# Kernel tuning notes

Measured on AMD Instinct MI355X. Metric: run time of the kernel, lower is better.

## Reference

```python
import jax, jax.numpy as jnp
import numpy as np


def setup_inputs() -> dict:
    key = jax.random.key(0)
    ks = jax.random.split(key, 6)
    D, k, r = 4096, 16, 32  # embed_dim, low_rank_dimension, 2*low_rank_dimension
    B, S = 4, 4096
    return {
        "base": jax.random.normal(ks[0], (B, S, D), dtype=jnp.float32),
        "lora_A": jax.random.normal(ks[1], (k, D), dtype=jnp.float32),
        "lora_E": jax.random.normal(ks[2], (r, 1), dtype=jnp.float32),
        "lora_B": jax.random.normal(ks[3], (r, k), dtype=jnp.float32),
        "lora_aa": jax.random.normal(ks[4], (k, r), dtype=jnp.float32),
        "lora_bb": jax.random.normal(ks[5], (D, k), dtype=jnp.float32),
    }


def reference(base, lora_A, lora_E, lora_B, lora_aa, lora_bb):
    # Original math: base + base @ (A.T @ B.T @ diag(E) @ aa.T @ bb.T)
    #   result1 = A.T @ B.T  -> [D, r]
    #   result2 = aa.T @ bb.T -> [r, D]
    # Efficient equivalent: keep it low-rank; never build the [D, D] matrix
    # or the explicit diag. diag(E) @ result2 == E * result2 (row scaling).
    e = lora_E.reshape(-1)                              # [r]
    t = jnp.einsum('bsd,kd->bsk', base, lora_A)         # [B,S,k]  (base @ A.T)
    t = jnp.einsum('bsk,rk->bsr', t, lora_B)            # [B,S,r]  (.. @ B.T)
    t = t * e                                           # diag(E) scaling
    t = jnp.einsum('bsr,kr->bsk', t, lora_aa)           # [B,S,k]  (.. @ aa.T)
    delta = jnp.einsum('bsk,dk->bsd', t, lora_bb)       # [B,S,D]  (.. @ bb.T)
    return (base + delta).astype(base.dtype)
```

## Files before the change

### kernel.cpp

```cpp
#include <hip/hip_runtime.h>
#include <hip/hip_bf16.h>


#define D_DIM 4096
#define K_LR 16
#define R_LR 32
#define ROWS 64
#define NW 16
#define WWIN 256
#define DC 32
#define NCH (WWIN / DC)

typedef float f32x4 __attribute__((ext_vector_type(4)));

__global__ void __launch_bounds__(256) prep_kernel(const float* __restrict__ A,
                                                   const float* __restrict__ E,
                                                   const float* __restrict__ Bm,
                                                   const float* __restrict__ aa,
                                                   float* __restrict__ A2t) {
    __shared__ float Ms[K_LR][K_LR];
    const int t = threadIdx.x;
    {
        const int k = t >> 4, kp = t & 15;
        float s = 0.f;
        #pragma unroll
        for (int r = 0; r < R_LR; ++r)
            s += Bm[r * K_LR + k] * E[r] * aa[kp * R_LR + r];
        Ms[k][kp] = s;
    }
    __syncthreads();
    const int d = blockIdx.x * 256 + t;
    float acc[K_LR];
    #pragma unroll
    for (int kp = 0; kp < K_LR; ++kp) acc[kp] = 0.f;
    #pragma unroll
    for (int k = 0; k < K_LR; ++k) {
        const float a = A[k * D_DIM + d];
        #pragma unroll
        for (int kp = 0; kp < K_LR; ++kp) acc[kp] = fmaf(a, Ms[k][kp], acc[kp]);
    }
    #pragma unroll
    for (int kq = 0; kq < 4; ++kq) {
        f32x4 v = { acc[kq*4+0], acc[kq*4+1], acc[kq*4+2], acc[kq*4+3] };
        *(f32x4*)(A2t + (size_t)d * K_LR + kq * 4) = v;
    }
}

union ShA {
    float stage[NW][ROWS][DC];
    float tred[NW][ROWS][K_LR];
};

__global__ void __launch_bounds__(1024) fused_kernel(const float* __restrict__ base,
                                                     const float* __restrict__ A2t,
                                                     const float* __restrict__ bb,
                                                     float* __restrict__ out, int N) {
    __shared__ ShA sh;
    __shared__ float tfin[ROWS][K_LR];
    const int tid  = threadIdx.x;
    const int lane = tid & 63;
    const int wv   = __builtin_amdgcn_readfirstlane(tid >> 6);
    const int r0   = blockIdx.x * ROWS;

    {
        const int a = lane >> 3;
        const int b = lane & 7;
        const int d0 = wv * WWIN;
        char* wbase = (char*)&sh.stage[wv][0][0];
        const int swz_w = 16 * (b ^ a);
        const int swz_r = (lane & 7) << 4;

        float acc[K_LR];
        #pragma unroll
        for (int k = 0; k < K_LR; ++k) acc[k] = 0.f;

        f32x4 st[8];
        #pragma unroll
        for (int i = 0; i < 8; ++i)
            st[i] = *(const f32x4*)(base + (size_t)(r0 + i*8 + a) * D_DIM + d0 + 4*b);

        for (int c = 0; c < NCH; ++c) {
            #pragma unroll
            for (int i = 0; i < 8; ++i)
                *(f32x4*)(wbase + (i*8 + a) * 128 + swz_w) = st[i];
            if (c + 1 < NCH) {
                const int dcn = d0 + (c + 1) * DC;
                #pragma unroll
                for (int i = 0; i < 8; ++i)
                    st[i] = *(const f32x4*)(base + (size_t)(r0 + i*8 + a) * D_DIM + dcn + 4*b);
            }
            const int dc = d0 + c * DC;
            #pragma unroll
            for (int j = 0; j < DC/4; ++j) {
                const f32x4 b4 = *(const f32x4*)(wbase + lane * 128 + ((16*j) ^ swz_r));
                const float* a2p = A2t + (size_t)(dc + 4*j) * K_LR;
                #pragma unroll
                for (int jj = 0; jj < 4; ++jj) {
                    const float bv = b4[jj];
                    #pragma unroll
                    for (int k = 0; k < K_LR; ++k)
                        acc[k] = fmaf(bv, a2p[jj * K_LR + k], acc[k]);
                }
            }
        }
        __syncthreads();
        #pragma unroll
        for (int kq = 0; kq < 4; ++kq) {
            f32x4 v = { acc[kq*4+0], acc[kq*4+1], acc[kq*4+2], acc[kq*4+3] };
            *(f32x4*)(&sh.tred[wv][lane][kq * 4]) = v;
        }
    }
    __syncthreads();
    {
        const int r = tid >> 4, k = tid & 15;
        float s = 0.f;
        #pragma unroll
        for (int w = 0; w < NW; ++w)
            s += sh.tred[w][r][k];
        tfin[r][k] = s;
    }
    __syncthreads();

    {
        const int cbase = tid * 4;
        f32x4 bbr[4][4];
        #pragma unroll
        for (int q = 0; q < 4; ++q)
            #pragma unroll
            for (int kq = 0; kq < 4; ++kq)
                bbr[q][kq] = *(const f32x4*)(bb + (size_t)(cbase + q) * K_LR + kq * 4);

        #pragma unroll 2
        for (int r = 0; r < ROWS; ++r) {
            f32x4 t16[4];
            #pragma unroll
            for (int kq = 0; kq < 4; ++kq)
                t16[kq] = *(const f32x4*)(&tfin[r][kq * 4]);

            const size_t row = (size_t)(r0 + r);
            const f32x4 bv = *(const f32x4*)(base + row * D_DIM + cbase);
            f32x4 ov;
            #pragma unroll
            for (int q = 0; q < 4; ++q) {
                float o = bv[q];
                #pragma unroll
                for (int k = 0; k < K_LR; ++k)
                    o = fmaf(t16[k >> 2][k & 3], bbr[q][k >> 2][k & 3], o);
                ov[q] = o;
            }
            __builtin_nontemporal_store(ov, (f32x4*)(out + row * D_DIM + cbase));
        }
    }
}

extern "C" void kernel_launch(void* const* d_in, const int* in_sizes, int n_in,
                              void* d_out, int out_size, void* d_ws, size_t ws_size,
                              hipStream_t stream) {
    const float* base = (const float*)d_in[0];
    const float* A    = (const float*)d_in[1];
    const float* E    = (const float*)d_in[2];
    const float* Bm   = (const float*)d_in[3];
    const float* aa   = (const float*)d_in[4];
    const float* bb   = (const float*)d_in[5];
    float* out = (float*)d_out;
    const int N = in_sizes[0] / D_DIM;

    float* A2t = (float*)d_ws;

    prep_kernel<<<D_DIM / 256, 256, 0, stream>>>(A, E, Bm, aa, A2t);
    fused_kernel<<<N / ROWS, 1024, 0, stream>>>(base, A2t, bb, out, N);
}
```

Before: 147.5 us.

## Halve rows per block and split rank across lane halves in projection

Reshapes the fused kernel to 512-thread blocks covering 32 rows, so each wave handles a 512-column window in 64-wide chunks. In the projection, each lane now owns one row and half of the 16 rank outputs, using vector loads of A2t instead of scalar loads. The bb expansion loops over two 2048-column windows. The aim is lower register pressure, higher occupancy (launch bounds 512,4) and less redundant A2t traffic per lane, at the cost of each lane reading more staged base values from LDS and a new swizzle pattern.

```diff
diff --git a/kernel.cpp b/kernel.cpp
--- a/kernel.cpp
+++ b/kernel.cpp
@@ -5,11 +5,12 @@
 #define D_DIM 4096
 #define K_LR 16
 #define R_LR 32
-#define ROWS 64
-#define NW 16
-#define WWIN 256
-#define DC 32
+#define ROWS 32
+#define NW 8
+#define WWIN 512
+#define DC 64
 #define NCH (WWIN / DC)
+#define BWIN 2048
 
 typedef float f32x4 __attribute__((ext_vector_type(4)));
 
@@ -51,10 +52,10 @@
     float tred[NW][ROWS][K_LR];
 };
 
-__global__ void __launch_bounds__(1024) fused_kernel(const float* __restrict__ base,
-                                                     const float* __restrict__ A2t,
-                                                     const float* __restrict__ bb,
-                                                     float* __restrict__ out, int N) {
+__global__ void __launch_bounds__(512, 4) fused_kernel(const float* __restrict__ base,
+                                                       const float* __restrict__ A2t,
+                                                       const float* __restrict__ bb,
+                                                       float* __restrict__ out, int N) {
     __shared__ ShA sh;
     __shared__ float tfin[ROWS][K_LR];
     const int tid  = threadIdx.x;
@@ -63,52 +64,51 @@
     const int r0   = blockIdx.x * ROWS;
 
     {
-        const int a = lane >> 3;
-        const int b = lane & 7;
+        const int c4 = lane & 15;
+        const int rg = lane >> 4;
+        const int row = lane & 31;
+        const int kh  = lane >> 5;
+        const int rmask = row & 15;
         const int d0 = wv * WWIN;
         char* wbase = (char*)&sh.stage[wv][0][0];
-        const int swz_w = 16 * (b ^ a);
-        const int swz_r = (lane & 7) << 4;
 
-        float acc[K_LR];
-        #pragma unroll
-        for (int k = 0; k < K_LR; ++k) acc[k] = 0.f;
+        f32x4 acc0 = {0.f, 0.f, 0.f, 0.f};
+        f32x4 acc1 = {0.f, 0.f, 0.f, 0.f};
 
         f32x4 st[8];
         #pragma unroll
         for (int i = 0; i < 8; ++i)
-            st[i] = *(const f32x4*)(base + (size_t)(r0 + i*8 + a) * D_DIM + d0 + 4*b);
+            st[i] = *(const f32x4*)(base + (size_t)(r0 + i*4 + rg) * D_DIM + d0 + c4*4);
 
         for (int c = 0; c < NCH; ++c) {
             #pragma unroll
-            for (int i = 0; i < 8; ++i)
-                *(f32x4*)(wbase + (i*8 + a) * 128 + swz_w) = st[i];
+            for (int i = 0; i < 8; ++i) {
+                const int wr = i*4 + rg;
+                *(f32x4*)(wbase + wr * 256 + ((c4 ^ (wr & 15)) << 4)) = st[i];
+            }
             if (c + 1 < NCH) {
                 const int dcn = d0 + (c + 1) * DC;
                 #pragma unroll
                 for (int i = 0; i < 8; ++i)
-                    st[i] = *(const f32x4*)(base + (size_t)(r0 + i*8 + a) * D_DIM + dcn + 4*b);
+                    st[i] = *(const f32x4*)(base + (size_t)(r0 + i*4 + rg) * D_DIM + dcn + c4*4);
             }
             const int dc = d0 + c * DC;
             #pragma unroll
-            for (int j = 0; j < DC/4; ++j) {
-                const f32x4 b4 = *(const f32x4*)(wbase + lane * 128 + ((16*j) ^ swz_r));
-                const float* a2p = A2t + (size_t)(dc + 4*j) * K_LR;
+            for (int j = 0; j < 16; ++j) {
+                const f32x4 b4 = *(const f32x4*)(wbase + row * 256 + ((j ^ rmask) << 4));
                 #pragma unroll
                 for (int jj = 0; jj < 4; ++jj) {
-                    const float bv = b4[jj];
-                    #pragma unroll
-                    for (int k = 0; k < K_LR; ++k)
-                        acc[k] = fmaf(bv, a2p[jj * K_LR + k], acc[k]);
+                    const float* ap = A2t + (size_t)(dc + j*4 + jj) * K_LR + kh * 8;
+                    const f32x4 a0 = *(const f32x4*)(ap);
+                    const f32x4 a1 = *(const f32x4*)(ap + 4);
+                    acc0 += b4[jj] * a0;
+                    acc1 += b4[jj] * a1;
                 }
             }
         }
         __syncthreads();
-        #pragma unroll
-        for (int kq = 0; kq < 4; ++kq) {
-            f32x4 v = { acc[kq*4+0], acc[kq*4+1], acc[kq*4+2], acc[kq*4+3] };
-            *(f32x4*)(&sh.tred[wv][lane][kq * 4]) = v;
-        }
+        *(f32x4*)(&sh.tred[wv][row][kh * 8 + 0]) = acc0;
+        *(f32x4*)(&sh.tred[wv][row][kh * 8 + 4]) = acc1;
     }
     __syncthreads();
     {
@@ -121,8 +121,9 @@
     }
     __syncthreads();
 
-    {
-        const int cbase = tid * 4;
+    #pragma unroll
+    for (int win = 0; win < D_DIM / BWIN; ++win) {
+        const int cbase = win * BWIN + tid * 4;
         f32x4 bbr[4][4];
         #pragma unroll
         for (int q = 0; q < 4; ++q)
@@ -168,5 +169,5 @@
     float* A2t = (float*)d_ws;
 
     prep_kernel<<<D_DIM / 256, 256, 0, stream>>>(A, E, Bm, aa, A2t);
-    fused_kernel<<<N / ROWS, 1024, 0, stream>>>(base, A2t, bb, out, N);
+    fused_kernel<<<N / ROWS, 512, 0, stream>>>(base, A2t, bb, out, N);
 }
```

Result: slower. 265.0 us (+79.6%).
